# Kernel tuning notes

Hardware: AMD Instinct MI355X
Metric: run time of the kernel (lower is better)

## Reference

```python
import jax, jax.numpy as jnp
import numpy as np

GRID_SIZE = 0.04   # matches init_kwargs grid_size
AXIS_CAP = 32      # max voxel bins per axis (1/0.04 = 25 < 32); keeps keys in int32 range


def setup_inputs() -> dict:
    key = jax.random.key(0)
    k1, k2 = jax.random.split(key)
    N, C = 1_000_000, 64
    coord = jax.random.uniform(k1, (N, 3), dtype=jnp.float32)   # points in unit cube
    feat = jax.random.normal(k2, (N, C), dtype=jnp.float32)
    # cumulative per-batch point counts (pointops offset convention), 4 equal batches
    offset = jnp.array([N // 4, N // 2, 3 * N // 4, N], dtype=jnp.int32)
    return {"coord": coord, "feat": feat, "offset": offset}


def reference(coord, feat, offset):
    N = coord.shape[0]
    B = offset.shape[0]
    # batch id per point from cumulative offsets
    batch = jnp.searchsorted(offset, jnp.arange(N, dtype=offset.dtype), side='right')  # [N]
    batch = batch.astype(jnp.int32)
    # voxelize_helper: start = per-batch min coord (start=None path)
    start = jax.ops.segment_min(coord, batch, num_segments=B)            # [B,3]
    vox = jnp.floor((coord - start[batch]) / GRID_SIZE).astype(jnp.int32)  # [N,3]
    # fused (batch, voxel) key; batches never share keys
    vkey = ((batch * AXIS_CAP + vox[:, 0]) * AXIS_CAP + vox[:, 1]) * AXIS_CAP + vox[:, 2]
    # sorted cluster indices + CSR-style segment ids
    order = jnp.argsort(vkey)                                            # sorted_cluster_indices
    skey = vkey[order]
    new_seg = jnp.concatenate([jnp.zeros((1,), jnp.int32),
                               (skey[1:] != skey[:-1]).astype(jnp.int32)])
    seg = jnp.cumsum(new_seg)                                            # [N] segment id per sorted point
    n_vox = seg[-1] + 1                                                  # actual number of voxels (traced)
    # segment_csr(coord[order], reduce='mean')
    counts = jax.ops.segment_sum(jnp.ones((N,), coord.dtype), seg, num_segments=N)  # [N] padded
    coord_out = jax.ops.segment_sum(coord[order], seg, num_segments=N) / jnp.maximum(counts, 1.0)[:, None]
    # segment_csr(feat[order], reduce='max')
    feat_out = jax.ops.segment_max(feat[order], seg, num_segments=N)
    valid = jnp.arange(N) < n_vox                                        # [N] pad mask
    coord_out = jnp.where(valid[:, None], coord_out, 0.0)
    feat_out = jnp.where(valid[:, None], feat_out, 0.0)
    # batch[idx_ptr[:-1]] -> batch of first point in each segment, then batch2offset
    batch_out = jax.ops.segment_min(batch[order], seg, num_segments=N)
    batch_out = jnp.where(valid, batch_out, B)                           # padded rows -> bucket B
    per_batch = jax.ops.segment_sum(jnp.ones((N,), jnp.int32), batch_out, num_segments=B + 1)[:B]
    offset_out = jnp.cumsum(per_batch)                                   # [B]
    # outputs padded to N rows; first n_vox rows are the real voxels
    return coord_out, feat_out, offset_out, n_vox
```

## Files before the change

kernel.cpp:

```cpp
#include <hip/hip_runtime.h>
#include <hip/hip_bf16.h>
#include <cstdint>

#define AXIS_CAP 32
#define GRID_SIZE_F 0.04f
#define BINS_PER_BATCH (AXIS_CAP * AXIS_CAP * AXIS_CAP)
#define SCAN_TPB 256
#define BINS_PER_THREAD 4
#define BINS_PER_BLOCK (SCAN_TPB * BINS_PER_THREAD)
#define KC_PPT 4

typedef float f32x4 __attribute__((ext_vector_type(4)));
typedef uint32_t u32x2 __attribute__((ext_vector_type(2)));

__device__ __forceinline__ int point_batch(int i, const int* offs, int B) {
    int b = 0;
    for (int k = 0; k < B; ++k) b += (offs[k] <= i);
    return b;
}

__global__ void init_kernel(uint32_t* binCount, int nbins, int* startBits, int B) {
    int i = blockIdx.x * blockDim.x + threadIdx.x;
    int stride = gridDim.x * blockDim.x;
    for (int v = i; v < nbins; v += stride) binCount[v] = 0;
    if (i < 3 * B) startBits[i] = 0x7F800000;
}

__global__ __launch_bounds__(256) void batch_min4_kernel(
        const float* __restrict__ coord, const int* __restrict__ offs,
        int B, int N, int* __restrict__ startBits) {
    __shared__ int smin[12];
    if (threadIdx.x < 12) smin[threadIdx.x] = 0x7F800000;
    __syncthreads();

    int o0 = offs[0];
    int o1 = (B > 1) ? offs[1] : o0;
    int o2 = (B > 2) ? offs[2] : o1;

    float m[4][3];
#pragma unroll
    for (int bb = 0; bb < 4; ++bb)
#pragma unroll
        for (int d = 0; d < 3; ++d) m[bb][d] = INFINITY;

    int gid = blockIdx.x * blockDim.x + threadIdx.x;
    int stride = gridDim.x * blockDim.x;
    for (int i = gid; i < N; i += stride) {
        float x = coord[(size_t)i * 3 + 0];
        float y = coord[(size_t)i * 3 + 1];
        float z = coord[(size_t)i * 3 + 2];
        int b = (i >= o0) + (i >= o1) + (i >= o2);
#pragma unroll
        for (int bb = 0; bb < 4; ++bb) {
            bool sel = (bb == b);
            m[bb][0] = fminf(m[bb][0], sel ? x : INFINITY);
            m[bb][1] = fminf(m[bb][1], sel ? y : INFINITY);
            m[bb][2] = fminf(m[bb][2], sel ? z : INFINITY);
        }
    }

#pragma unroll
    for (int bb = 0; bb < 4; ++bb)
#pragma unroll
        for (int d = 0; d < 3; ++d) {
            float v = m[bb][d];
            for (int off = 32; off > 0; off >>= 1)
                v = fminf(v, __shfl_xor(v, off));
            m[bb][d] = v;
        }

    if ((threadIdx.x & 63) == 0) {
#pragma unroll
        for (int bb = 0; bb < 4; ++bb)
#pragma unroll
            for (int d = 0; d < 3; ++d)
                atomicMin(&smin[bb * 3 + d], __float_as_int(m[bb][d]));
    }
    __syncthreads();
    if (threadIdx.x < 12 && (threadIdx.x / 3) < B)
        atomicMin(&startBits[threadIdx.x], smin[threadIdx.x]);
}

__global__ void batch_min_generic_kernel(const float* __restrict__ coord,
                                         const int* __restrict__ offs,
                                         int B, int N, int* startBits) {
    int i = blockIdx.x * blockDim.x + threadIdx.x;
    if (i >= N) return;
    int b = point_batch(i, offs, B);
    for (int d = 0; d < 3; ++d) {
        float c = coord[(size_t)i * 3 + d];
        atomicMin(&startBits[b * 3 + d], __float_as_int(c));
    }
}

__global__ __launch_bounds__(256) void keys_count4_kernel(
        const float* __restrict__ coord, const int* __restrict__ offs,
        const int* __restrict__ startBits, int B, int N,
        u32x2* __restrict__ kr, uint32_t* __restrict__ binCount) {
    int o0 = offs[0];
    int o1 = (B > 1) ? offs[1] : o0;
    int o2 = (B > 2) ? offs[2] : o1;
    float s00 = __int_as_float(startBits[0]);
    float s01 = __int_as_float(startBits[1]);
    float s02 = __int_as_float(startBits[2]);
    float s10 = (B > 1) ? __int_as_float(startBits[3]) : 0.f;
    float s11 = (B > 1) ? __int_as_float(startBits[4]) : 0.f;
    float s12 = (B > 1) ? __int_as_float(startBits[5]) : 0.f;
    float s20 = (B > 2) ? __int_as_float(startBits[6]) : 0.f;
    float s21 = (B > 2) ? __int_as_float(startBits[7]) : 0.f;
    float s22 = (B > 2) ? __int_as_float(startBits[8]) : 0.f;
    float s30 = (B > 3) ? __int_as_float(startBits[9]) : 0.f;
    float s31 = (B > 3) ? __int_as_float(startBits[10]) : 0.f;
    float s32 = (B > 3) ? __int_as_float(startBits[11]) : 0.f;

    int i0 = blockIdx.x * (256 * KC_PPT) + threadIdx.x;
#pragma unroll
    for (int j = 0; j < KC_PPT; ++j) {
        int i = i0 + j * 256;
        if (i >= N) continue;
        float x = coord[(size_t)i * 3 + 0];
        float y = coord[(size_t)i * 3 + 1];
        float z = coord[(size_t)i * 3 + 2];
        int b = (i >= o0) + (i >= o1) + (i >= o2);
        float sx = (b == 0) ? s00 : (b == 1) ? s10 : (b == 2) ? s20 : s30;
        float sy = (b == 0) ? s01 : (b == 1) ? s11 : (b == 2) ? s21 : s31;
        float sz = (b == 0) ? s02 : (b == 1) ? s12 : (b == 2) ? s22 : s32;
        int vx = (int)floorf((x - sx) / GRID_SIZE_F);
        int vy = (int)floorf((y - sy) / GRID_SIZE_F);
        int vz = (int)floorf((z - sz) / GRID_SIZE_F);
        vx = vx < 0 ? 0 : (vx > AXIS_CAP - 1 ? AXIS_CAP - 1 : vx);
        vy = vy < 0 ? 0 : (vy > AXIS_CAP - 1 ? AXIS_CAP - 1 : vy);
        vz = vz < 0 ? 0 : (vz > AXIS_CAP - 1 ? AXIS_CAP - 1 : vz);
        uint32_t key = ((uint32_t)b * AXIS_CAP + vx) * AXIS_CAP * AXIS_CAP
                     + (uint32_t)vy * AXIS_CAP + vz;
        uint32_t r = atomicAdd(&binCount[key], 1u);
        u32x2 kv = {key, r};
        kr[i] = kv;
    }
}

__global__ void keys_count_generic_kernel(
        const float* __restrict__ coord, const int* __restrict__ offs,
        const int* __restrict__ startBits, int B, int N,
        u32x2* __restrict__ kr, uint32_t* __restrict__ binCount) {
    int i = blockIdx.x * blockDim.x + threadIdx.x;
    if (i >= N) return;
    int b = point_batch(i, offs, B);
    int v[3];
    for (int d = 0; d < 3; ++d) {
        float s = __int_as_float(startBits[b * 3 + d]);
        float q = (coord[(size_t)i * 3 + d] - s) / GRID_SIZE_F;
        int vi = (int)floorf(q);
        vi = vi < 0 ? 0 : (vi > AXIS_CAP - 1 ? AXIS_CAP - 1 : vi);
        v[d] = vi;
    }
    uint32_t key = ((uint32_t)b * AXIS_CAP + v[0]) * AXIS_CAP * AXIS_CAP
                 + (uint32_t)v[1] * AXIS_CAP + v[2];
    uint32_t r = atomicAdd(&binCount[key], 1u);
    u32x2 kv = {key, r};
    kr[i] = kv;
}

__global__ void scan1_kernel(const uint32_t* __restrict__ binCount,
                             uint32_t* __restrict__ binStart,
                             uint32_t* __restrict__ binSeg,
                             uint32_t* __restrict__ blockCnt,
                             uint32_t* __restrict__ blockOcc) {
    __shared__ uint32_t sC[SCAN_TPB], sO[SCAN_TPB];
    int t = threadIdx.x;
    int base = blockIdx.x * BINS_PER_BLOCK + t * BINS_PER_THREAD;
    uint32_t c[BINS_PER_THREAD];
    uint32_t tc = 0, to = 0;
#pragma unroll
    for (int j = 0; j < BINS_PER_THREAD; ++j) {
        c[j] = binCount[base + j];
        tc += c[j];
        to += (c[j] > 0u);
    }
    sC[t] = tc; sO[t] = to;
    __syncthreads();
    for (int off = 1; off < SCAN_TPB; off <<= 1) {
        uint32_t a = 0, b2 = 0;
        if (t >= off) { a = sC[t - off]; b2 = sO[t - off]; }
        __syncthreads();
        sC[t] += a; sO[t] += b2;
        __syncthreads();
    }
    uint32_t exC = sC[t] - tc;
    uint32_t exO = sO[t] - to;
#pragma unroll
    for (int j = 0; j < BINS_PER_THREAD; ++j) {
        binStart[base + j] = exC;
        binSeg[base + j] = exO;
        exC += c[j];
        exO += (c[j] > 0u);
    }
    if (t == SCAN_TPB - 1) {
        blockCnt[blockIdx.x] = sC[t];
        blockOcc[blockIdx.x] = sO[t];
    }
}

__global__ void scan2_kernel(uint32_t* blockCnt, uint32_t* blockOcc,
                             uint32_t* totals, int nb) {
    __shared__ uint32_t sC[SCAN_TPB], sO[SCAN_TPB];
    int t = threadIdx.x;
    uint32_t c = (t < nb) ? blockCnt[t] : 0u;
    uint32_t o = (t < nb) ? blockOcc[t] : 0u;
    sC[t] = c; sO[t] = o;
    __syncthreads();
    for (int off = 1; off < SCAN_TPB; off <<= 1) {
        uint32_t a = 0, b2 = 0;
        if (t >= off) { a = sC[t - off]; b2 = sO[t - off]; }
        __syncthreads();
        sC[t] += a; sO[t] += b2;
        __syncthreads();
    }
    if (t < nb) { blockCnt[t] = sC[t] - c; blockOcc[t] = sO[t] - o; }
    if (t == SCAN_TPB - 1) { totals[0] = sO[t]; totals[1] = sC[t]; }
}

__global__ void scan3_kernel(const uint32_t* __restrict__ binCount,
                             uint32_t* __restrict__ binStart,
                             uint32_t* __restrict__ binSeg,
                             uint32_t* __restrict__ occList,
                             const uint32_t* __restrict__ blockCnt,
                             const uint32_t* __restrict__ blockOcc) {
    int t = threadIdx.x;
    int base = blockIdx.x * BINS_PER_BLOCK + t * BINS_PER_THREAD;
    uint32_t oc = blockCnt[blockIdx.x];
    uint32_t oo = blockOcc[blockIdx.x];
#pragma unroll
    for (int j = 0; j < BINS_PER_THREAD; ++j) {
        uint32_t seg = binSeg[base + j] + oo;
        binStart[base + j] += oc;
        binSeg[base + j] = seg;
        if (binCount[base + j] > 0u) occList[seg] = (uint32_t)(base + j);
    }
}

__global__ void scatter_kernel(const u32x2* __restrict__ kr,
                               const uint32_t* __restrict__ binStart,
                               uint32_t* __restrict__ pointIdx, int N,
                               const uint32_t* __restrict__ binSeg,
                               const uint32_t* __restrict__ totals,
                               float* __restrict__ out, int B, int C) {
    int i = blockIdx.x * blockDim.x + threadIdx.x;
    if (blockIdx.x == 0 && threadIdx.x <= (unsigned)B) {
        uint32_t nvox = totals[0];
        float* tail = out + (size_t)N * 3 + (size_t)N * C;
        if (threadIdx.x < (unsigned)B) {
            uint32_t v = (threadIdx.x == (unsigned)(B - 1))
                             ? nvox
                             : binSeg[(size_t)(threadIdx.x + 1) * BINS_PER_BATCH];
            tail[threadIdx.x] = (float)v;
        }
        if (threadIdx.x == 0) tail[B] = (float)nvox;
    }
    if (i >= N) return;
    u32x2 k = __builtin_nontemporal_load(&kr[i]);
    pointIdx[binStart[k.x] + k.y] = (uint32_t)i;
}

__global__ __launch_bounds__(256) void reduce_kernel(
        const float* __restrict__ coord, const float* __restrict__ feat,
        const uint32_t* __restrict__ binCount,
        const uint32_t* __restrict__ binStart,
        const uint32_t* __restrict__ occList,
        const uint32_t* __restrict__ pointIdx,
        const uint32_t* __restrict__ totals,
        float* __restrict__ out, int N, int C) {
    int wid = (blockIdx.x << 2) + (threadIdx.x >> 6);
    int lane = threadIdx.x & 63;
    uint32_t nvox = totals[0];
    float* feat_out = out + (size_t)N * 3;

    if ((uint32_t)wid < nvox) {
        int bin = (int)occList[wid];
        uint32_t cnt = binCount[bin];
        uint32_t st = binStart[bin];
        uint32_t seg = (uint32_t)wid;
        float sx = 0.f, sy = 0.f, sz = 0.f;

        if (C == 64) {
            float m = -INFINITY;
            for (uint32_t base = 0; base < cnt; base += 64) {
                uint32_t nchunk = min(64u, cnt - base);
                bool valid = lane < (int)nchunk;
                uint32_t myIdx = valid ? pointIdx[st + base + lane] : 0u;
                if (valid) {
                    const float* cp = coord + (size_t)myIdx * 3;
                    sx += cp[0]; sy += cp[1]; sz += cp[2];
                }
                for (uint32_t p = 0; p < nchunk; p += 16) {
                    float v[16];
#pragma unroll
                    for (int j = 0; j < 16; ++j) {
                        uint32_t pp = min(p + (uint32_t)j, nchunk - 1u);
                        uint32_t idx = __shfl(myIdx, (int)pp);
                        v[j] = feat[(size_t)idx * 64 + lane];
                    }
#pragma unroll
                    for (int s = 1; s < 16; s <<= 1)
#pragma unroll
                        for (int j = 0; j < 16; j += 2 * s)
                            v[j] = fmaxf(v[j], v[j + s]);
                    m = fmaxf(m, v[0]);
                }
            }
            __builtin_nontemporal_store(m, &feat_out[(size_t)seg * 64 + lane]);
        } else {
            for (uint32_t p = lane; p < cnt; p += 64) {
                uint32_t idx = pointIdx[st + p];
                sx += coord[(size_t)idx * 3 + 0];
                sy += coord[(size_t)idx * 3 + 1];
                sz += coord[(size_t)idx * 3 + 2];
            }
            for (int c = lane; c < C; c += 64) {
                float m = -INFINITY;
                for (uint32_t p = 0; p < cnt; ++p) {
                    uint32_t idx = pointIdx[st + p];
                    m = fmaxf(m, feat[(size_t)idx * C + c]);
                }
                feat_out[(size_t)seg * C + c] = m;
            }
        }

        for (int off = 32; off > 0; off >>= 1) {
            sx += __shfl_xor(sx, off);
            sy += __shfl_xor(sy, off);
            sz += __shfl_xor(sz, off);
        }
        if (lane == 0) {
            float inv = 1.0f / (float)cnt;
            out[(size_t)seg * 3 + 0] = sx * inv;
            out[(size_t)seg * 3 + 1] = sy * inv;
            out[(size_t)seg * 3 + 2] = sz * inv;
        }
    }

    uint32_t tid = (uint32_t)blockIdx.x * blockDim.x + threadIdx.x;
    uint32_t nthreads = (uint32_t)gridDim.x * blockDim.x;
    uint32_t rows = (uint32_t)N - nvox;
    if ((C & 3) == 0) {
        f32x4 z4 = {0.f, 0.f, 0.f, 0.f};
        uint32_t quadsTotal = rows * (uint32_t)(C >> 2);
        f32x4* padBase = (f32x4*)(feat_out + (size_t)nvox * C);
        for (uint32_t q = tid; q < quadsTotal; q += nthreads)
            __builtin_nontemporal_store(z4, &padBase[q]);
    } else {
        uint32_t eTotal = rows * (uint32_t)C;
        float* padBase = feat_out + (size_t)nvox * C;
        for (uint32_t e = tid; e < eTotal; e += nthreads)
            __builtin_nontemporal_store(0.f, &padBase[e]);
    }
    {
        uint32_t cTotal = rows * 3u;
        float* cBase = out + (size_t)nvox * 3;
        for (uint32_t e = tid; e < cTotal; e += nthreads)
            __builtin_nontemporal_store(0.f, &cBase[e]);
    }
}

extern "C" void kernel_launch(void* const* d_in, const int* in_sizes, int n_in,
                              void* d_out, int out_size, void* d_ws, size_t ws_size,
                              hipStream_t stream) {
    const float* coord = (const float*)d_in[0];
    const float* feat  = (const float*)d_in[1];
    const int*   offs  = (const int*)d_in[2];
    float* out = (float*)d_out;

    int N = in_sizes[0] / 3;
    int C = in_sizes[1] / N;
    int B = in_sizes[2];
    int NBINS = B * BINS_PER_BATCH;
    int NB1 = NBINS / BINS_PER_BLOCK;

    uint8_t* w = (uint8_t*)d_ws;
    uint32_t* binCount = (uint32_t*)w;              w += (size_t)NBINS * 4;
    uint32_t* binStart = (uint32_t*)w;              w += (size_t)NBINS * 4;
    uint32_t* binSeg   = (uint32_t*)w;              w += (size_t)NBINS * 4;
    uint32_t* occList  = (uint32_t*)w;              w += (size_t)NBINS * 4;
    uint32_t* blockCnt = (uint32_t*)w;              w += (size_t)NB1 * 4;
    uint32_t* blockOcc = (uint32_t*)w;              w += (size_t)NB1 * 4;
    uint32_t* totals   = (uint32_t*)w;              w += 2 * 4;
    int*      startBits= (int*)w;                   w += (size_t)3 * B * 4 + 8;
    u32x2*    kr       = (u32x2*)w;                 w += (size_t)N * 8;
    uint32_t* pointIdx = (uint32_t*)w;

    int ptBlocks = (N + 255) / 256;
    int kcBlocks = (N + 256 * KC_PPT - 1) / (256 * KC_PPT);

    init_kernel<<<512, 256, 0, stream>>>(binCount, NBINS, startBits, B);
    if (B <= 4) {
        batch_min4_kernel<<<1024, 256, 0, stream>>>(coord, offs, B, N, startBits);
        keys_count4_kernel<<<kcBlocks, 256, 0, stream>>>(coord, offs, startBits,
                                                         B, N, kr, binCount);
    } else {
        batch_min_generic_kernel<<<ptBlocks, 256, 0, stream>>>(coord, offs, B, N,
                                                               startBits);
        keys_count_generic_kernel<<<ptBlocks, 256, 0, stream>>>(coord, offs,
                                                                startBits, B, N,
                                                                kr, binCount);
    }
    scan1_kernel<<<NB1, SCAN_TPB, 0, stream>>>(binCount, binStart, binSeg,
                                               blockCnt, blockOcc);
    scan2_kernel<<<1, SCAN_TPB, 0, stream>>>(blockCnt, blockOcc, totals, NB1);
    scan3_kernel<<<NB1, SCAN_TPB, 0, stream>>>(binCount, binStart, binSeg,
                                               occList, blockCnt, blockOcc);
    scatter_kernel<<<ptBlocks, 256, 0, stream>>>(kr, binStart, pointIdx, N,
                                                 binSeg, totals, out, B, C);
    reduce_kernel<<<NBINS / 4, 256, 0, stream>>>(coord, feat, binCount, binStart,
                                                 occList, pointIdx, totals, out,
                                                 N, C);
}
```

Measured before the change: 188.8 us.

## Recompute voxel keys in scatter and pack coords with indices in sorted records

Keys-count now stores only a per-point rank, and scatter recomputes each voxel key from the coordinates rather than reading a stored key/rank pair. Scatter writes a 16-byte record of (x, y, z, index) into sorted position, so the reduce kernel reads coordinates contiguously instead of gathering them through point indices. Reduce also becomes a grid-stride loop with a fixed block count instead of one wave per possible bin. In exchange, scatter rereads coordinates and writes 16 bytes per point where it used to write 4.

```diff
diff --git a/kernel.cpp b/kernel.cpp
--- a/kernel.cpp
+++ b/kernel.cpp
@@ -9,6 +9,7 @@
 #define BINS_PER_THREAD 4
 #define BINS_PER_BLOCK (SCAN_TPB * BINS_PER_THREAD)
 #define KC_PPT 4
+#define RED_BLOCKS 16384
 
 typedef float f32x4 __attribute__((ext_vector_type(4)));
 typedef uint32_t u32x2 __attribute__((ext_vector_type(2)));
@@ -17,6 +18,19 @@
     int b = 0;
     for (int k = 0; k < B; ++k) b += (offs[k] <= i);
     return b;
+}
+
+__device__ __forceinline__ uint32_t voxel_key(float x, float y, float z,
+                                              float sx, float sy, float sz,
+                                              int b) {
+    int vx = (int)floorf((x - sx) / GRID_SIZE_F);
+    int vy = (int)floorf((y - sy) / GRID_SIZE_F);
+    int vz = (int)floorf((z - sz) / GRID_SIZE_F);
+    vx = vx < 0 ? 0 : (vx > AXIS_CAP - 1 ? AXIS_CAP - 1 : vx);
+    vy = vy < 0 ? 0 : (vy > AXIS_CAP - 1 ? AXIS_CAP - 1 : vy);
+    vz = vz < 0 ? 0 : (vz > AXIS_CAP - 1 ? AXIS_CAP - 1 : vz);
+    return ((uint32_t)b * AXIS_CAP + vx) * AXIS_CAP * AXIS_CAP
+         + (uint32_t)vy * AXIS_CAP + vz;
 }
 
 __global__ void init_kernel(uint32_t* binCount, int nbins, int* startBits, int B) {
@@ -96,7 +110,7 @@
 __global__ __launch_bounds__(256) void keys_count4_kernel(
         const float* __restrict__ coord, const int* __restrict__ offs,
         const int* __restrict__ startBits, int B, int N,
-        u32x2* __restrict__ kr, uint32_t* __restrict__ binCount) {
+        uint32_t* __restrict__ rank, uint32_t* __restrict__ binCount) {
     int o0 = offs[0];
     int o1 = (B > 1) ? offs[1] : o0;
     int o2 = (B > 2) ? offs[2] : o1;
@@ -125,40 +139,26 @@
         float sx = (b == 0) ? s00 : (b == 1) ? s10 : (b == 2) ? s20 : s30;
         float sy = (b == 0) ? s01 : (b == 1) ? s11 : (b == 2) ? s21 : s31;
         float sz = (b == 0) ? s02 : (b == 1) ? s12 : (b == 2) ? s22 : s32;
-        int vx = (int)floorf((x - sx) / GRID_SIZE_F);
-        int vy = (int)floorf((y - sy) / GRID_SIZE_F);
-        int vz = (int)floorf((z - sz) / GRID_SIZE_F);
-        vx = vx < 0 ? 0 : (vx > AXIS_CAP - 1 ? AXIS_CAP - 1 : vx);
-        vy = vy < 0 ? 0 : (vy > AXIS_CAP - 1 ? AXIS_CAP - 1 : vy);
-        vz = vz < 0 ? 0 : (vz > AXIS_CAP - 1 ? AXIS_CAP - 1 : vz);
-        uint32_t key = ((uint32_t)b * AXIS_CAP + vx) * AXIS_CAP * AXIS_CAP
-                     + (uint32_t)vy * AXIS_CAP + vz;
-        uint32_t r = atomicAdd(&binCount[key], 1u);
-        u32x2 kv = {key, r};
-        kr[i] = kv;
+        uint32_t key = voxel_key(x, y, z, sx, sy, sz, b);
+        rank[i] = atomicAdd(&binCount[key], 1u);
     }
 }
 
 __global__ void keys_count_generic_kernel(
         const float* __restrict__ coord, const int* __restrict__ offs,
         const int* __restrict__ startBits, int B, int N,
-        u32x2* __restrict__ kr, uint32_t* __restrict__ binCount) {
+        uint32_t* __restrict__ rank, uint32_t* __restrict__ binCount) {
     int i = blockIdx.x * blockDim.x + threadIdx.x;
     if (i >= N) return;
     int b = point_batch(i, offs, B);
-    int v[3];
-    for (int d = 0; d < 3; ++d) {
-        float s = __int_as_float(startBits[b * 3 + d]);
-        float q = (coord[(size_t)i * 3 + d] - s) / GRID_SIZE_F;
-        int vi = (int)floorf(q);
-        vi = vi < 0 ? 0 : (vi > AXIS_CAP - 1 ? AXIS_CAP - 1 : vi);
-        v[d] = vi;
-    }
-    uint32_t key = ((uint32_t)b * AXIS_CAP + v[0]) * AXIS_CAP * AXIS_CAP
-                 + (uint32_t)v[1] * AXIS_CAP + v[2];
-    uint32_t r = atomicAdd(&binCount[key], 1u);
-    u32x2 kv = {key, r};
-    kr[i] = kv;
+    float x = coord[(size_t)i * 3 + 0];
+    float y = coord[(size_t)i * 3 + 1];
+    float z = coord[(size_t)i * 3 + 2];
+    uint32_t key = voxel_key(x, y, z,
+                             __int_as_float(startBits[b * 3 + 0]),
+                             __int_as_float(startBits[b * 3 + 1]),
+                             __int_as_float(startBits[b * 3 + 2]), b);
+    rank[i] = atomicAdd(&binCount[key], 1u);
 }
 
 __global__ void scan1_kernel(const uint32_t* __restrict__ binCount,
@@ -239,12 +239,70 @@
     }
 }
 
-__global__ void scatter_kernel(const u32x2* __restrict__ kr,
-                               const uint32_t* __restrict__ binStart,
-                               uint32_t* __restrict__ pointIdx, int N,
-                               const uint32_t* __restrict__ binSeg,
-                               const uint32_t* __restrict__ totals,
-                               float* __restrict__ out, int B, int C) {
+__global__ __launch_bounds__(256) void scatter4_kernel(
+        const float* __restrict__ coord, const int* __restrict__ offs,
+        const int* __restrict__ startBits,
+        const uint32_t* __restrict__ rank,
+        const uint32_t* __restrict__ binStart,
+        f32x4* __restrict__ records, int B, int N,
+        const uint32_t* __restrict__ binSeg,
+        const uint32_t* __restrict__ totals,
+        float* __restrict__ out, int C) {
+    if (blockIdx.x == 0 && threadIdx.x <= (unsigned)B) {
+        uint32_t nvox = totals[0];
+        float* tail = out + (size_t)N * 3 + (size_t)N * C;
+        if (threadIdx.x < (unsigned)B) {
+            uint32_t v = (threadIdx.x == (unsigned)(B - 1))
+                             ? nvox
+                             : binSeg[(size_t)(threadIdx.x + 1) * BINS_PER_BATCH];
+            tail[threadIdx.x] = (float)v;
+        }
+        if (threadIdx.x == 0) tail[B] = (float)nvox;
+    }
+    int o0 = offs[0];
+    int o1 = (B > 1) ? offs[1] : o0;
+    int o2 = (B > 2) ? offs[2] : o1;
+    float s00 = __int_as_float(startBits[0]);
+    float s01 = __int_as_float(startBits[1]);
+    float s02 = __int_as_float(startBits[2]);
+    float s10 = (B > 1) ? __int_as_float(startBits[3]) : 0.f;
+    float s11 = (B > 1) ? __int_as_float(startBits[4]) : 0.f;
+    float s12 = (B > 1) ? __int_as_float(startBits[5]) : 0.f;
+    float s20 = (B > 2) ? __int_as_float(startBits[6]) : 0.f;
+    float s21 = (B > 2) ? __int_as_float(startBits[7]) : 0.f;
+    float s22 = (B > 2) ? __int_as_float(startBits[8]) : 0.f;
+    float s30 = (B > 3) ? __int_as_float(startBits[9]) : 0.f;
+    float s31 = (B > 3) ? __int_as_float(startBits[10]) : 0.f;
+    float s32 = (B > 3) ? __int_as_float(startBits[11]) : 0.f;
+
+    int i0 = blockIdx.x * (256 * KC_PPT) + threadIdx.x;
+#pragma unroll
+    for (int j = 0; j < KC_PPT; ++j) {
+        int i = i0 + j * 256;
+        if (i >= N) continue;
+        float x = coord[(size_t)i * 3 + 0];
+        float y = coord[(size_t)i * 3 + 1];
+        float z = coord[(size_t)i * 3 + 2];
+        int b = (i >= o0) + (i >= o1) + (i >= o2);
+        float sx = (b == 0) ? s00 : (b == 1) ? s10 : (b == 2) ? s20 : s30;
+        float sy = (b == 0) ? s01 : (b == 1) ? s11 : (b == 2) ? s21 : s31;
+        float sz = (b == 0) ? s02 : (b == 1) ? s12 : (b == 2) ? s22 : s32;
+        uint32_t key = voxel_key(x, y, z, sx, sy, sz, b);
+        uint32_t pos = binStart[key] + __builtin_nontemporal_load(&rank[i]);
+        f32x4 rec = {x, y, z, __uint_as_float((uint32_t)i)};
+        records[pos] = rec;
+    }
+}
+
+__global__ void scatter_generic_kernel(
+        const float* __restrict__ coord, const int* __restrict__ offs,
+        const int* __restrict__ startBits,
+        const uint32_t* __restrict__ rank,
+        const uint32_t* __restrict__ binStart,
+        f32x4* __restrict__ records, int B, int N,
+        const uint32_t* __restrict__ binSeg,
+        const uint32_t* __restrict__ totals,
+        float* __restrict__ out, int C) {
     int i = blockIdx.x * blockDim.x + threadIdx.x;
     if (blockIdx.x == 0 && threadIdx.x <= (unsigned)B) {
         uint32_t nvox = totals[0];
@@ -258,28 +316,37 @@
         if (threadIdx.x == 0) tail[B] = (float)nvox;
     }
     if (i >= N) return;
-    u32x2 k = __builtin_nontemporal_load(&kr[i]);
-    pointIdx[binStart[k.x] + k.y] = (uint32_t)i;
+    int b = point_batch(i, offs, B);
+    float x = coord[(size_t)i * 3 + 0];
+    float y = coord[(size_t)i * 3 + 1];
+    float z = coord[(size_t)i * 3 + 2];
+    uint32_t key = voxel_key(x, y, z,
+                             __int_as_float(startBits[b * 3 + 0]),
+                             __int_as_float(startBits[b * 3 + 1]),
+                             __int_as_float(startBits[b * 3 + 2]), b);
+    uint32_t pos = binStart[key] + rank[i];
+    f32x4 rec = {x, y, z, __uint_as_float((uint32_t)i)};
+    records[pos] = rec;
 }
 
 __global__ __launch_bounds__(256) void reduce_kernel(
-        const float* __restrict__ coord, const float* __restrict__ feat,
+        const float* __restrict__ feat,
         const uint32_t* __restrict__ binCount,
         const uint32_t* __restrict__ binStart,
         const uint32_t* __restrict__ occList,
-        const uint32_t* __restrict__ pointIdx,
+        const f32x4* __restrict__ records,
         const uint32_t* __restrict__ totals,
         float* __restrict__ out, int N, int C) {
     int wid = (blockIdx.x << 2) + (threadIdx.x >> 6);
     int lane = threadIdx.x & 63;
+    int totalWaves = gridDim.x << 2;
     uint32_t nvox = totals[0];
     float* feat_out = out + (size_t)N * 3;
 
-    if ((uint32_t)wid < nvox) {
-        int bin = (int)occList[wid];
+    for (uint32_t seg = (uint32_t)wid; seg < nvox; seg += (uint32_t)totalWaves) {
+        int bin = (int)occList[seg];
         uint32_t cnt = binCount[bin];
         uint32_t st = binStart[bin];
-        uint32_t seg = (uint32_t)wid;
         float sx = 0.f, sy = 0.f, sz = 0.f;
 
         if (C == 64) {
@@ -287,11 +354,10 @@
             for (uint32_t base = 0; base < cnt; base += 64) {
                 uint32_t nchunk = min(64u, cnt - base);
                 bool valid = lane < (int)nchunk;
-                uint32_t myIdx = valid ? pointIdx[st + base + lane] : 0u;
-                if (valid) {
-                    const float* cp = coord + (size_t)myIdx * 3;
-                    sx += cp[0]; sy += cp[1]; sz += cp[2];
-                }
+                f32x4 rec = {0.f, 0.f, 0.f, 0.f};
+                if (valid) rec = records[st + base + lane];
+                uint32_t myIdx = __float_as_uint(rec.w);
+                if (valid) { sx += rec.x; sy += rec.y; sz += rec.z; }
                 for (uint32_t p = 0; p < nchunk; p += 16) {
                     float v[16];
 #pragma unroll
@@ -311,15 +377,13 @@
             __builtin_nontemporal_store(m, &feat_out[(size_t)seg * 64 + lane]);
         } else {
             for (uint32_t p = lane; p < cnt; p += 64) {
-                uint32_t idx = pointIdx[st + p];
-                sx += coord[(size_t)idx * 3 + 0];
-                sy += coord[(size_t)idx * 3 + 1];
-                sz += coord[(size_t)idx * 3 + 2];
+                f32x4 rec = records[st + p];
+                sx += rec.x; sy += rec.y; sz += rec.z;
             }
             for (int c = lane; c < C; c += 64) {
                 float m = -INFINITY;
                 for (uint32_t p = 0; p < cnt; ++p) {
-                    uint32_t idx = pointIdx[st + p];
+                    uint32_t idx = __float_as_uint(records[st + p].w);
                     m = fmaxf(m, feat[(size_t)idx * C + c]);
                 }
                 feat_out[(size_t)seg * C + c] = m;
@@ -385,8 +449,10 @@
     uint32_t* blockOcc = (uint32_t*)w;              w += (size_t)NB1 * 4;
     uint32_t* totals   = (uint32_t*)w;              w += 2 * 4;
     int*      startBits= (int*)w;                   w += (size_t)3 * B * 4 + 8;
-    u32x2*    kr       = (u32x2*)w;                 w += (size_t)N * 8;
-    uint32_t* pointIdx = (uint32_t*)w;
+    w = (uint8_t*)(((uintptr_t)w + 15) & ~(uintptr_t)15);
+    uint32_t* rank     = (uint32_t*)w;              w += (size_t)N * 4;
+    w = (uint8_t*)(((uintptr_t)w + 15) & ~(uintptr_t)15);
+    f32x4*    records  = (f32x4*)w;
 
     int ptBlocks = (N + 255) / 256;
     int kcBlocks = (N + 256 * KC_PPT - 1) / (256 * KC_PPT);
@@ -395,22 +461,32 @@
     if (B <= 4) {
         batch_min4_kernel<<<1024, 256, 0, stream>>>(coord, offs, B, N, startBits);
         keys_count4_kernel<<<kcBlocks, 256, 0, stream>>>(coord, offs, startBits,
-                                                         B, N, kr, binCount);
+                                                         B, N, rank, binCount);
     } else {
         batch_min_generic_kernel<<<ptBlocks, 256, 0, stream>>>(coord, offs, B, N,
                                                                startBits);
         keys_count_generic_kernel<<<ptBlocks, 256, 0, stream>>>(coord, offs,
                                                                 startBits, B, N,
-                                                                kr, binCount);
+                                                                rank, binCount);
     }
     scan1_kernel<<<NB1, SCAN_TPB, 0, stream>>>(binCount, binStart, binSeg,
                                                blockCnt, blockOcc);
     scan2_kernel<<<1, SCAN_TPB, 0, stream>>>(blockCnt, blockOcc, totals, NB1);
     scan3_kernel<<<NB1, SCAN_TPB, 0, stream>>>(binCount, binStart, binSeg,
                                                occList, blockCnt, blockOcc);
-    scatter_kernel<<<ptBlocks, 256, 0, stream>>>(kr, binStart, pointIdx, N,
-                                                 binSeg, totals, out, B, C);
-    reduce_kernel<<<NBINS / 4, 256, 0, stream>>>(coord, feat, binCount, binStart,
-                                                 occList, pointIdx, totals, out,
-                                                 N, C);
-}
+    if (B <= 4) {
+        scatter4_kernel<<<kcBlocks, 256, 0, stream>>>(coord, offs, startBits,
+                                                      rank, binStart, records,
+                                                      B, N, binSeg, totals,
+                                                      out, C);
+    } else {
+        scatter_generic_kernel<<<ptBlocks, 256, 0, stream>>>(coord, offs,
+                                                             startBits, rank,
+                                                             binStart, records,
+                                                             B, N, binSeg,
+                                                             totals, out, C);
+    }
+    reduce_kernel<<<RED_BLOCKS, 256, 0, stream>>>(feat, binCount, binStart,
+                                                  occList, records, totals,
+                                                  out, N, C);
+}
```

Result: slower. 196.3 us (+4.0%).
